# Kernel tuning notes

Measured on AMD Instinct MI355X. Metric: run time of the kernel, lower is better.

## Reference

```python
import jax, jax.numpy as jnp
import numpy as np
from jax import lax

EPS = 1e-5
B, NA, NE, NAL = 1024, 10, 10, 9

def qbn(x):
    # QBN_RM1d: divide by RMS of detached input over all dims but last
    xd = lax.stop_gradient(x)
    mean2 = jnp.mean((xd * xd).reshape(-1, xd.shape[-1]), axis=0)
    return x / jnpp_sqrt(mean2) if False else x / jnp.sqrt(mean2 + EPS)

def qrelu(x):
    # Qrelu1d: scale each 2-vector (axis -2) by mod/max(1,mod), mod from detached x
    xd = lax.stop_gradient(x)
    mod = jnp.sqrt(jnp.sum(xd * xd, axis=-2))
    coeff = mod / jnp.maximum(1.0, mod)
    return x * coeff[..., None, :]

def rcn(x, Ws):
    for W in Ws:
        x = qrelu(qbn(x @ W))
    return x

def qmerge(x):
    return jnp.sum(x * x, axis=-2)

def qmaxpool(x):
    # x: [B,A,N,2,C]; pick per-channel entity with max squared 2-norm
    xd = lax.stop_gradient(x)
    mod = jnp.sum(xd * xd, axis=-2)            # [B,A,N,C]
    idx = jnp.argmax(mod, axis=-2)             # [B,A,C]
    idxb = jnp.broadcast_to(idx[:, :, None, None, :], x.shape[:2] + (1,) + x.shape[-2:])
    return jnp.take_along_axis(x, idxb, axis=-3)[:, :, 0]   # [B,A,2,C]

def build_vec(feats, own_vec):
    # feats: [B,A,n,9]; own_vec: [B,A,2,11]
    pos = feats[..., 2:4][..., None]                          # [B,A,n,2,1]
    pos_mod = jnp.sqrt(jnp.sum(pos * pos, axis=-2))           # [B,A,n,1]
    other = jnp.concatenate([feats[..., :2], feats[..., 4:]], axis=-1)  # [B,A,n,7]
    other_mod = jnp.sqrt(2.0 * other * other)                 # repeat-2 then 2-norm = sqrt(2*x^2)
    mask = pos_mod == 0.0
    denom = jnp.where(mask, 1.0, pos_mod)
    coff = jnp.where(mask, 0.0, other_mod / denom)[..., None, :]   # [B,A,n,1,7]
    vec = pos * coff                                           # [B,A,n,2,7]
    own_mod = jnp.sqrt(jnp.sum(own_vec * own_vec, axis=-2))[:, :, None, :]  # [B,A,1,11]
    own_coff = jnp.where(mask, 0.0, own_mod / denom)[..., None, :]          # [B,A,n,1,11]
    own_vecf = pos * own_coff                                  # [B,A,n,2,11]
    return jnp.concatenate([pos, vec, own_vecf], axis=-1)      # [B,A,n,2,19]

def setup_inputs() -> dict:
    key = jax.random.key(0)
    ks = jax.random.split(key, 32)
    s = 0.1
    inp = {
        'own_feats':   jax.random.normal(ks[0], (B, NA, 11), jnp.float32),
        'enemy_feats': jax.random.normal(ks[1], (B, NA, NE, 9), jnp.float32),
        'ally_feats':  jax.random.normal(ks[2], (B, NA, NAL, 9), jnp.float32),
        'W_e1': jax.random.normal(ks[3], (19, 64), jnp.float32) * s,
        'W_e2': jax.random.normal(ks[4], (64, 64), jnp.float32) * s,
        'W_a1': jax.random.normal(ks[5], (19, 64), jnp.float32) * s,
        'W_a2': jax.random.normal(ks[6], (64, 64), jnp.float32) * s,
        'W_f1': jax.random.normal(ks[7], (64, 64), jnp.float32) * s,
        'W_f2': jax.random.normal(ks[8], (64, 64), jnp.float32) * s,
        'W_ie1': jax.random.normal(ks[9], (128, 64), jnp.float32) * s,
        'W_ie2': jax.random.normal(ks[10], (64, 64), jnp.float32) * s,
        'W_ie3': jax.random.normal(ks[11], (64, 1), jnp.float32) * s,
        'W_ia1': jax.random.normal(ks[12], (128, 64), jnp.float32) * s,
        'W_ia2': jax.random.normal(ks[13], (64, 64), jnp.float32) * s,
        'W_ia3': jax.random.normal(ks[14], (64, 1), jnp.float32) * s,
        'W_oa1': jax.random.normal(ks[15], (64, 64), jnp.float32) * s,
        'b_oa1': jnp.zeros((64,), jnp.float32),
        'W_oa2': jax.random.normal(ks[16], (64, 3), jnp.float32) * s,
        'b_oa2': jnp.zeros((3,), jnp.float32),
        'W_at1': jax.random.normal(ks[17], (128, 128), jnp.float32) * s,
        'b_at1': jnp.zeros((128,), jnp.float32),
        'W_at2': jax.random.normal(ks[18], (128, 64), jnp.float32) * s,
        'b_at2': jnp.zeros((64,), jnp.float32),
        'W_at3': jax.random.normal(ks[19], (64, 1), jnp.float32) * s,
        'b_at3': jnp.zeros((1,), jnp.float32),
    }
    return inp

def reference(own_feats, enemy_feats, ally_feats,
              W_e1, W_e2, W_a1, W_a2, W_f1, W_f2,
              W_ie1, W_ie2, W_ie3, W_ia1, W_ia2, W_ia3,
              W_oa1, b_oa1, W_oa2, b_oa2,
              W_at1, b_at1, W_at2, b_at2, W_at3, b_at3):
    Bc = own_feats.shape[0]
    own_vec = jnp.repeat(own_feats[:, :, None, :], 2, axis=2)        # [B,A,2,11]
    ev = build_vec(enemy_feats, own_vec)                              # [B,A,10,2,19]
    av = build_vec(ally_feats, own_vec)                               # [B,A,9,2,19]
    e_rc = rcn(ev, (W_e1, W_e2))                                      # [B,A,10,2,64]
    e_scalar = qmerge(e_rc)                                           # [B,A,10,64]
    a_rc = rcn(av, (W_a1, W_a2))                                      # [B,A,9,2,64]
    all_rc = jnp.concatenate([e_rc, a_rc], axis=-3)                   # [B,A,19,2,64]
    vf = rcn(qmaxpool(all_rc), (W_f1, W_f2))                          # [B,A,2,64]
    vrep = jnp.broadcast_to(vf[:, :, None], (Bc, NA, NE, 2, 64))
    cat = jnp.concatenate([vrep, e_rc], axis=-1)                      # [B,A,10,2,128]
    e_imp = rcn(cat, (W_ie1, W_ie2, W_ie3))                           # [B,A,10,2,1]
    a_imp = rcn(cat, (W_ia1, W_ia2, W_ia3))                           # (orig code also uses enemy feats here)
    move_vec = jnp.sum(jnp.concatenate([e_imp, a_imp], axis=-3), axis=-3)  # [B,A,2,1]
    sf = qmerge(vf)                                                   # [B,A,64]
    oaq = jax.nn.relu(sf @ W_oa1 + b_oa1) @ W_oa2 + b_oa2             # [B,A,3]
    mmq = oaq[:, :, 2:3]
    up = mmq + move_vec[:, :, 1, :]
    down = mmq - move_vec[:, :, 1, :]
    right = mmq + move_vec[:, :, 0, :]
    left = mmq - move_vec[:, :, 0, :]
    move_q = jnp.concatenate([up, down, right, left], axis=-1)        # [B,A,4]
    sfr = jnp.broadcast_to(sf[:, :, None, :], (Bc, NA, NE, 64))
    atf = jnp.concatenate([sfr, e_scalar], axis=-1)                   # [B,A,10,128]
    h = jax.nn.relu(atf @ W_at1 + b_at1)
    h = jax.nn.relu(h @ W_at2 + b_at2)
    aq = (h @ W_at3 + b_at3)[..., 0]                                  # [B,A,10]
    return jnp.concatenate([oaq[:, :, 0:2], move_q, aq], axis=-1)     # [B,A,16]
```

## Files before the change

### kernel.cpp

```cpp
#include <hip/hip_runtime.h>
#include <math.h>

#define BATCH 1024
#define NA 10
#define NEN 10
#define NALY 9
#define NAG (BATCH*NA)
#define NEE (NAG*NEN)
#define NAE (NAG*NALY)
#define EPSF 1e-5f

#define DOFF_SE1 0
#define DOFF_SE2 1024
#define DOFF_SA1 2048
#define DOFF_SA2 3072
#define DOFF_SF1 4096
#define DOFF_SF2 5120
#define DOFF_SIE1 6144
#define DOFF_SIE2 7168
#define DOFF_SIA1 8192
#define DOFF_SIA2 9216
#define DOFF_SIE3 10240
#define DOFF_SIA3 10368
#define NDOUBLES 16384

#define NBLK_BE (NEE/8)
#define NBLK_BA (NAE/8)
#define NBLK_PE (NEE/16)
#define NBLK_PA (NAE/16)

__device__ __forceinline__ double sum16vd(const double* __restrict__ S, int ch) {
    double s = 0.0;
#pragma unroll
    for (int r = 0; r < 16; ++r) s += S[r*64 + ch];
    return s;
}
__device__ __forceinline__ double sum16sd8(const double* __restrict__ S) {
    double s = 0.0;
#pragma unroll
    for (int r = 0; r < 16; ++r) s += S[r*8];
    return s;
}
__device__ __forceinline__ float qbn_s(const double* __restrict__ S, int ch, double invRows) {
    float m = (float)(sum16vd(S, ch)*invRows);
    return sqrtf(m + EPSF);
}
__device__ __forceinline__ void red_to_S(const double* red, double* S, int bid, int tid) {
    if (tid < 64) {
        double v = red[tid] + red[tid+64] + red[tid+128] + red[tid+192];
        atomicAdd(&S[(bid & 15)*64 + tid], v);
    }
}
__device__ __forceinline__ float pair_m2(float x0, float x1) {
    return __fadd_rn(__fmul_rn(x0,x0), __fmul_rn(x1,x1));
}

__global__ __launch_bounds__(256) void k_build_both(
    const float* __restrict__ ef, const float* __restrict__ af,
    const float* __restrict__ own,
    const float* __restrict__ We1, const float* __restrict__ Wa1,
    float* __restrict__ XE, float* __restrict__ XA,
    double* __restrict__ SE1, double* __restrict__ SA1)
{
    bool isA = (blockIdx.x >= NBLK_BE);
    int blk = isA ? (blockIdx.x - NBLK_BE) : blockIdx.x;
    const float* feats = isA ? af : ef;
    const float* W1    = isA ? Wa1 : We1;
    float* X           = isA ? XA : XE;
    double* S1         = isA ? SA1 : SE1;
    int nEntPerAgent   = isA ? NALY : NEN;

    __shared__ float wlds[19*64];
    __shared__ float gpc[16][19];
    __shared__ double red[256];
    int tid = threadIdx.x;
    for (int i = tid; i < 19*64; i += 256) wlds[i] = W1[i];
    if (tid < 152) {
        int el = tid / 19, chg = tid % 19;
        int ent = blk*8 + el;
        const float* f = feats + (size_t)ent*9;
        int agent = ent / nEntPerAgent;
        float px = f[2], py = f[3];
        float pm = sqrtf(__fadd_rn(__fmul_rn(px,px), __fmul_rn(py,py)));
        float val;
        if (chg == 0) val = 1.f;
        else if (chg < 8) {
            int j = chg - 1;
            int fi = (j < 2) ? j : (j + 2);
            float o = f[fi];
            float om = sqrtf(__fmul_rn(__fmul_rn(2.0f,o),o));
            val = (pm == 0.f) ? 0.f : __fdiv_rn(om, pm);
        } else {
            float o = own[(size_t)agent*11 + (chg-8)];
            float t = __fmul_rn(o,o);
            float om = sqrtf(__fadd_rn(t,t));
            val = (pm == 0.f) ? 0.f : __fdiv_rn(om, pm);
        }
        gpc[el*2 + 0][chg] = __fmul_rn(px, val);
        gpc[el*2 + 1][chg] = __fmul_rn(py, val);
    }
    __syncthreads();
    int l = tid >> 7, c = (tid >> 6) & 1, ch = tid & 63;
    float wreg[19];
#pragma unroll
    for (int k = 0; k < 19; ++k) wreg[k] = wlds[k*64+ch];
    double lr = 0.0;
#pragma unroll
    for (int i = 0; i < 4; ++i) {
        int el = l + 2*i;
        int ent = blk*8 + el;
        int row = el*2 + c;
        float acc = 0.f;
#pragma unroll
        for (int k = 18; k >= 0; --k) {
            acc = fmaf(gpc[row][k], wreg[k], acc);
        }
        X[(size_t)ent*128 + c*64 + ch] = acc;
        lr += (double)acc * (double)acc;
    }
    red[tid] = lr;
    __syncthreads();
    red_to_S(red, S1, blk, tid);
}

__device__ __forceinline__ void pair_layer_body(
    float* __restrict__ X, const double* __restrict__ Sin, double* __restrict__ Sout,
    const float* __restrict__ W, double invRows, int blk)
{
    __shared__ float wlds[4096];
    __shared__ float ybuf[16][132];
    __shared__ float ss[64];
    __shared__ double dredw[4][64];
    int tid = threadIdx.x;
    for (int i = tid; i < 4096; i += 256) wlds[i] = W[i];
    if (tid < 64) ss[tid] = qbn_s(Sin, tid, invRows);
    __syncthreads();
    int rl = tid >> 4;
    int ch0 = (tid & 15) * 4;
    size_t row = (size_t)blk*16 + rl;
    float4 xv0 = *(const float4*)&X[row*128 + ch0];
    float4 xv1 = *(const float4*)&X[row*128 + 64 + ch0];
    {
        float xs0[4] = {xv0.x,xv0.y,xv0.z,xv0.w};
        float xs1[4] = {xv1.x,xv1.y,xv1.z,xv1.w};
        float y0[4], y1[4];
#pragma unroll
        for (int i = 0; i < 4; ++i) {
            float s = ss[ch0+i];
            float u0 = xs0[i]/s, u1 = xs1[i]/s;
            float mod = sqrtf(pair_m2(u0,u1));
            float cf = mod / fmaxf(1.f, mod);
            y0[i] = __fmul_rn(u0,cf);
            y1[i] = __fmul_rn(u1,cf);
        }
        *(float4*)&ybuf[rl][2*ch0]     = make_float4(y0[0],y1[0],y0[1],y1[1]);
        *(float4*)&ybuf[rl][2*ch0 + 4] = make_float4(y0[2],y1[2],y0[3],y1[3]);
    }
    __syncthreads();
    float a0[4] = {0.f,0.f,0.f,0.f};
    float a1[4] = {0.f,0.f,0.f,0.f};
#pragma unroll
    for (int k = 63; k >= 1; k -= 2) {
        float4 wk  = *(const float4*)&wlds[k*64 + ch0];
        float4 wk1 = *(const float4*)&wlds[(k-1)*64 + ch0];
        float4 y4  = *(const float4*)&ybuf[rl][2*k - 2];
        float wkv[4]  = {wk.x,wk.y,wk.z,wk.w};
        float wk1v[4] = {wk1.x,wk1.y,wk1.z,wk1.w};
#pragma unroll
        for (int i = 0; i < 4; ++i) {
            a0[i] = fmaf(y4.z, wkv[i], a0[i]);
            a1[i] = fmaf(y4.w, wkv[i], a1[i]);
        }
#pragma unroll
        for (int i = 0; i < 4; ++i) {
            a0[i] = fmaf(y4.x, wk1v[i], a0[i]);
            a1[i] = fmaf(y4.y, wk1v[i], a1[i]);
        }
    }
    *(float4*)&X[row*128 + ch0]      = make_float4(a0[0],a0[1],a0[2],a0[3]);
    *(float4*)&X[row*128 + 64 + ch0] = make_float4(a1[0],a1[1],a1[2],a1[3]);
    {
        int wv = tid >> 6;
#pragma unroll
        for (int i = 0; i < 4; ++i) {
            double d = (double)a0[i]*a0[i] + (double)a1[i]*a1[i];
            d += __shfl_xor(d, 16, 64);
            d += __shfl_xor(d, 32, 64);
            if ((tid & 48) == 0) dredw[wv][ch0+i] = d;
        }
    }
    __syncthreads();
    if (tid < 64) {
        double v = dredw[0][tid] + dredw[1][tid] + dredw[2][tid] + dredw[3][tid];
        atomicAdd(&Sout[(blk & 15)*64 + tid], v);
    }
}

__global__ __launch_bounds__(256) void k_pair_both(
    float* __restrict__ XE, const double* __restrict__ SE1, double* __restrict__ SE2,
    const float* __restrict__ We2, double invRe,
    float* __restrict__ XA, const double* __restrict__ SA1, double* __restrict__ SA2,
    const float* __restrict__ Wa2, double invRa)
{
    if (blockIdx.x < NBLK_PE)
        pair_layer_body(XE, SE1, SE2, We2, invRe, blockIdx.x);
    else
        pair_layer_body(XA, SA1, SA2, Wa2, invRa, blockIdx.x - NBLK_PE);
}

__global__ __launch_bounds__(256) void k_pair_layer(
    float* __restrict__ X, const double* __restrict__ Sin, double* __restrict__ Sout,
    const float* __restrict__ W, double invRows)
{
    pair_layer_body(X, Sin, Sout, W, invRows, blockIdx.x);
}

__global__ __launch_bounds__(256) void k_finalize_pair(
    float* __restrict__ X, const double* __restrict__ S2, double invRows,
    float* __restrict__ ESC)
{
    __shared__ float ss[64];
    if (threadIdx.x < 64) ss[threadIdx.x] = qbn_s(S2, threadIdx.x, invRows);
    int t = blockIdx.x*256 + threadIdx.x;
    int rl = t >> 4;
    int ch0 = (t & 15) * 4;
    size_t base    = (size_t)rl*64 + ch0;
    size_t partner = (size_t)(rl ^ 1)*64 + ch0;
    float4 xv  = *(const float4*)&X[base];
    float4 xov = *(const float4*)&X[partner];
    __syncthreads();
    float xs[4]  = {xv.x,xv.y,xv.z,xv.w};
    float xos[4] = {xov.x,xov.y,xov.z,xov.w};
    float r[4], esc[4];
    int c = rl & 1;
#pragma unroll
    for (int i = 0; i < 4; ++i) {
        float s = ss[ch0+i];
        float u  = xs[i]/s;
        float uo = xos[i]/s;
        float u0 = (c==0) ? u : uo, u1 = (c==0) ? uo : u;
        float mod = sqrtf(pair_m2(u0,u1));
        float cf = mod / fmaxf(1.f, mod);
        r[i] = __fmul_rn(u, cf);
        if (c == 0) {
            float y1v = __fmul_rn(uo, cf);
            esc[i] = pair_m2(r[i], y1v);
        }
    }
    *(float4*)&X[base] = make_float4(r[0],r[1],r[2],r[3]);
    if (c == 0) {
        int ent = rl >> 1;
        *(float4*)&ESC[(size_t)ent*64 + ch0] = make_float4(esc[0],esc[1],esc[2],esc[3]);
    }
}

__global__ __launch_bounds__(256) void k_pool_f1(
    const float* __restrict__ XE, const float* __restrict__ XAraw,
    const double* __restrict__ SA2, double invRa,
    const float* __restrict__ Wf1, float* __restrict__ F1, double* __restrict__ Sf1)
{
    __shared__ float wlds[4096];
    __shared__ float v[4][2][64];
    __shared__ float ssa[64];
    __shared__ double red[256];
    int tid = threadIdx.x;
    for (int i = tid; i < 4096; i += 256) wlds[i] = Wf1[i];
    if (tid < 64) ssa[tid] = qbn_s(SA2, tid, invRa);
    __syncthreads();
    int grp = tid>>6, ch = tid&63;
    int agent = blockIdx.x*4 + grp;
    float best = -1.f, v0 = 0.f, v1 = 0.f;
    for (int e = 0; e < NEN; ++e) {
        size_t b = (size_t)(agent*NEN+e)*128;
        float x0 = XE[b+ch], x1 = XE[b+64+ch];
        float m2 = pair_m2(x0,x1);
        if (m2 > best) { best = m2; v0 = x0; v1 = x1; }
    }
    float sa = ssa[ch];
    for (int l = 0; l < NALY; ++l) {
        size_t b = (size_t)(agent*NALY+l)*128;
        float r0 = XAraw[b+ch], r1 = XAraw[b+64+ch];
        float u0 = r0/sa, u1 = r1/sa;
        float modf = sqrtf(pair_m2(u0,u1));
        float cff = modf / fmaxf(1.f, modf);
        float x0 = __fmul_rn(u0,cff), x1 = __fmul_rn(u1,cff);
        float m2 = pair_m2(x0,x1);
        if (m2 > best) { best = m2; v0 = x0; v1 = x1; }
    }
    v[grp][0][ch] = v0; v[grp][1][ch] = v1;
    __syncthreads();
    float a0 = 0.f, a1 = 0.f;
#pragma unroll
    for (int k = 0; k < 64; ++k) {
        float w = wlds[k*64+ch];
        a0 = fmaf(v[grp][0][k], w, a0);
        a1 = fmaf(v[grp][1][k], w, a1);
    }
    F1[(size_t)agent*128+ch] = a0; F1[(size_t)agent*128+64+ch] = a1;
    red[tid] = (double)a0*a0 + (double)a1*a1;
    __syncthreads();
    red_to_S(red, Sf1, blockIdx.x, tid);
}

__global__ __launch_bounds__(256) void k_vf_vtop(
    float* __restrict__ F1, const double* __restrict__ Sf2,
    float* __restrict__ SFb,
    const float* __restrict__ Wie1, const float* __restrict__ Wia1,
    const float* __restrict__ Wat1, const float* __restrict__ bat1,
    float* __restrict__ VTie, float* __restrict__ VTia, double invRows)
{
    __shared__ float wie[4096];
    __shared__ float wia[4096];
    __shared__ float vf[4][2][64];
    __shared__ float sfv[4][64];
    int tid = threadIdx.x;
    for (int i = tid; i < 4096; i += 256) { wie[i] = Wie1[i]; wia[i] = Wia1[i]; }
    int grp = tid>>6, ch = tid&63;
    int agent = blockIdx.x*4 + grp;
    float x0 = F1[(size_t)agent*128+ch], x1 = F1[(size_t)agent*128+64+ch];
    float s = qbn_s(Sf2, ch, invRows);
    float u0 = x0/s, u1 = x1/s;
    float mod = sqrtf(pair_m2(u0,u1));
    float cf = mod / fmaxf(1.f, mod);
    float y0 = __fmul_rn(u0,cf), y1 = __fmul_rn(u1,cf);
    vf[grp][0][ch] = y0; vf[grp][1][ch] = y1;
    float sf = pair_m2(y0,y1);
    SFb[(size_t)agent*64+ch] = sf;
    sfv[grp][ch] = sf;
    __syncthreads();
    float a0=0.f,a1=0.f,b0=0.f,b1=0.f;
    float at0 = bat1[ch], at1 = bat1[64+ch];
#pragma unroll
    for (int k = 0; k < 64; ++k) {
        float f0 = vf[grp][0][k], f1 = vf[grp][1][k];
        a0 = fmaf(f0, wie[k*64+ch], a0); a1 = fmaf(f1, wie[k*64+ch], a1);
        b0 = fmaf(f0, wia[k*64+ch], b0); b1 = fmaf(f1, wia[k*64+ch], b1);
        float sv = sfv[grp][k];
        at0 = fmaf(sv, Wat1[k*128 + ch], at0);
        at1 = fmaf(sv, Wat1[k*128 + 64 + ch], at1);
    }
    VTie[(size_t)agent*128+ch] = a0; VTie[(size_t)agent*128+64+ch] = a1;
    VTia[(size_t)agent*128+ch] = b0; VTia[(size_t)agent*128+64+ch] = b1;
    F1[(size_t)agent*128+ch] = at0; F1[(size_t)agent*128+64+ch] = at1;
}

__global__ __launch_bounds__(256) void k_imp1(
    const float* __restrict__ XE, const float* __restrict__ VT,
    const float* __restrict__ W1, float* __restrict__ XI, double* __restrict__ S1)
{
    __shared__ float wlds[4096];
    __shared__ float xt[16][68];
    __shared__ double dredw[4][64];
    int tid = threadIdx.x;
    for (int i = tid; i < 4096; i += 256) wlds[i] = W1[4096 + i];
    {
        int r = tid >> 4;
        int kq = (tid & 15) * 4;
        float4 t4 = *(const float4*)&XE[(size_t)blockIdx.x*1024 + tid*4];
        *(float4*)&xt[r][kq] = t4;
    }
    __syncthreads();
    int rl = tid >> 4;
    int ch0 = (tid & 15) * 4;
    int ent = blockIdx.x*8 + (rl >> 1);
    int c = rl & 1;
    int agent = ent / NEN;
    float4 vt = *(const float4*)&VT[(size_t)agent*128 + c*64 + ch0];
    float acc[4] = {vt.x, vt.y, vt.z, vt.w};
#pragma unroll
    for (int k = 0; k < 64; k += 4) {
        float4 x4 = *(const float4*)&xt[rl][k];
        float xk[4] = {x4.x, x4.y, x4.z, x4.w};
#pragma unroll
        for (int kk = 0; kk < 4; ++kk) {
            float4 w4 = *(const float4*)&wlds[(k+kk)*64 + ch0];
            acc[0] = fmaf(xk[kk], w4.x, acc[0]);
            acc[1] = fmaf(xk[kk], w4.y, acc[1]);
            acc[2] = fmaf(xk[kk], w4.z, acc[2]);
            acc[3] = fmaf(xk[kk], w4.w, acc[3]);
        }
    }
    *(float4*)&XI[(size_t)ent*128 + c*64 + ch0] = make_float4(acc[0],acc[1],acc[2],acc[3]);
    {
        int wv = tid >> 6;
#pragma unroll
        for (int i = 0; i < 4; ++i) {
            double d = (double)acc[i]*acc[i];
            d += __shfl_xor(d, 16, 64);
            d += __shfl_xor(d, 32, 64);
            if ((tid & 48) == 0) dredw[wv][ch0+i] = d;
        }
    }
    __syncthreads();
    if (tid < 64) {
        double v = dredw[0][tid] + dredw[1][tid] + dredw[2][tid] + dredw[3][tid];
        atomicAdd(&S1[(blockIdx.x & 15)*64 + tid], v);
    }
}

__global__ __launch_bounds__(256) void k_imp3(
    const float* __restrict__ XI, const double* __restrict__ S2,
    const float* __restrict__ W3, float* __restrict__ Z, double* __restrict__ S3,
    double invRows)
{
    __shared__ float ss[64];
    __shared__ double red4[4];
    int tid = threadIdx.x; int grp = tid>>6, ch = tid&63;
    if (tid < 64) ss[tid] = qbn_s(S2, tid, invRows);
    __syncthreads();
    float s = ss[ch];
    double w3 = (double)W3[ch];
    double lr3 = 0.0;
#pragma unroll
    for (int i = 0; i < 4; ++i) {
        int ent = blockIdx.x*16 + grp + 4*i;
        float x0 = XI[(size_t)ent*128+ch], x1 = XI[(size_t)ent*128+64+ch];
        float u0 = x0/s, u1 = x1/s;
        float mod = sqrtf(pair_m2(u0,u1));
        float cf = mod / fmaxf(1.f, mod);
        double v0 = (double)__fmul_rn(u0,cf) * w3;
        double v1 = (double)__fmul_rn(u1,cf) * w3;
#pragma unroll
        for (int m = 1; m < 64; m <<= 1) { v0 += __shfl_xor(v0,m,64); v1 += __shfl_xor(v1,m,64); }
        if (ch == 0) {
            float z0 = (float)v0, z1 = (float)v1;
            Z[(size_t)ent*2] = z0; Z[(size_t)ent*2+1] = z1;
            lr3 += (double)z0*z0 + (double)z1*z1;
        }
    }
    if (ch == 0) red4[grp] = lr3;
    __syncthreads();
    if (tid == 0) atomicAdd(&S3[(blockIdx.x & 15)*8], red4[0]+red4[1]+red4[2]+red4[3]);
}

__global__ __launch_bounds__(256) void k_final_small(
    const float* __restrict__ Zie, const float* __restrict__ Zia,
    const double* __restrict__ Sie3, const double* __restrict__ Sia3,
    const float* __restrict__ SFb,
    const float* __restrict__ Woa1, const float* __restrict__ boa1,
    const float* __restrict__ Woa2, const float* __restrict__ boa2,
    float* __restrict__ out, double invRows)
{
    __shared__ float sflds[4][64];
    int tid = threadIdx.x; int grp = tid>>6, ch = tid&63;
    int agent = blockIdx.x*4 + grp;
    float sie = sqrtf((float)(sum16sd8(Sie3)*invRows) + EPSF);
    float sia = sqrtf((float)(sum16sd8(Sia3)*invRows) + EPSF);
    double pv0 = 0.0, pv1 = 0.0;
    if (ch < NEN) {
        int ent = agent*NEN + ch;
        float z0 = Zie[(size_t)ent*2]/sie, z1 = Zie[(size_t)ent*2+1]/sie;
        float mod = sqrtf(pair_m2(z0,z1)); float cf = mod/fmaxf(1.f,mod);
        pv0 = (double)__fmul_rn(z0,cf); pv1 = (double)__fmul_rn(z1,cf);
        z0 = Zia[(size_t)ent*2]/sia; z1 = Zia[(size_t)ent*2+1]/sia;
        mod = sqrtf(pair_m2(z0,z1)); cf = mod/fmaxf(1.f,mod);
        pv0 += (double)__fmul_rn(z0,cf); pv1 += (double)__fmul_rn(z1,cf);
    }
#pragma unroll
    for (int m = 1; m < 64; m <<= 1) { pv0 += __shfl_xor(pv0,m,64); pv1 += __shfl_xor(pv1,m,64); }
    sflds[grp][ch] = SFb[(size_t)agent*64+ch];
    __syncthreads();
    double hd = (double)boa1[ch];
#pragma unroll
    for (int k = 0; k < 64; ++k) hd += (double)sflds[grp][k]*(double)Woa1[k*64+ch];
    float h = fmaxf((float)hd, 0.f);
    double q0 = (double)h*(double)Woa2[ch*3+0];
    double q1 = (double)h*(double)Woa2[ch*3+1];
    double q2 = (double)h*(double)Woa2[ch*3+2];
#pragma unroll
    for (int m = 1; m < 64; m <<= 1) { q0 += __shfl_xor(q0,m,64); q1 += __shfl_xor(q1,m,64); q2 += __shfl_xor(q2,m,64); }
    if (ch == 0) {
        float oaq0 = (float)(q0 + (double)boa2[0]);
        float oaq1 = (float)(q1 + (double)boa2[1]);
        float mmq  = (float)(q2 + (double)boa2[2]);
        float mv0 = (float)pv0, mv1 = (float)pv1;
        float* o = out + (size_t)agent*16;
        o[0] = oaq0; o[1] = oaq1;
        o[2] = mmq + mv1; o[3] = mmq - mv1;
        o[4] = mmq + mv0; o[5] = mmq - mv0;
    }
}

__global__ __launch_bounds__(256) void k_attn(
    const float* __restrict__ ATtop, const float* __restrict__ ESC,
    const float* __restrict__ W1,
    const float* __restrict__ W2, const float* __restrict__ b2,
    const float* __restrict__ W3, const float* __restrict__ b3,
    float* __restrict__ out)
{
    __shared__ float escT[64][20];
    __shared__ float h1T[128][20];
    __shared__ float h2[16][68];
    int tid = threadIdx.x;
    int row0 = blockIdx.x*16;
#pragma unroll
    for (int i = 0; i < 4; ++i) {
        int idx = tid + i*256; int r = idx>>6; int j = idx&63;
        escT[j][r] = ESC[(size_t)(row0 + r)*64 + j];
    }
    __syncthreads();
    {
        int j = tid & 127, rr = tid >> 7;
        float acc[8];
#pragma unroll
        for (int r = 0; r < 8; ++r) {
            int ent = row0 + rr*8 + r; int agent = ent/NEN;
            acc[r] = ATtop[(size_t)agent*128 + j];
        }
#pragma unroll 8
        for (int k = 0; k < 64; ++k) {
            float w = W1[(64 + k)*128 + j];
            float4 a0 = *(const float4*)&escT[k][rr*8];
            float4 a1 = *(const float4*)&escT[k][rr*8 + 4];
            acc[0] = fmaf(a0.x, w, acc[0]);
            acc[1] = fmaf(a0.y, w, acc[1]);
            acc[2] = fmaf(a0.z, w, acc[2]);
            acc[3] = fmaf(a0.w, w, acc[3]);
            acc[4] = fmaf(a1.x, w, acc[4]);
            acc[5] = fmaf(a1.y, w, acc[5]);
            acc[6] = fmaf(a1.z, w, acc[6]);
            acc[7] = fmaf(a1.w, w, acc[7]);
        }
        float4 o0 = make_float4(fmaxf(acc[0],0.f), fmaxf(acc[1],0.f),
                                fmaxf(acc[2],0.f), fmaxf(acc[3],0.f));
        float4 o1 = make_float4(fmaxf(acc[4],0.f), fmaxf(acc[5],0.f),
                                fmaxf(acc[6],0.f), fmaxf(acc[7],0.f));
        *(float4*)&h1T[j][rr*8]     = o0;
        *(float4*)&h1T[j][rr*8 + 4] = o1;
    }
    __syncthreads();
    {
        int j2 = tid & 63, rr2 = tid >> 6;
        float bb = b2[j2];
        float acc[4] = {bb, bb, bb, bb};
#pragma unroll 8
        for (int k = 0; k < 128; ++k) {
            float w = W2[k*64 + j2];
            float4 p = *(const float4*)&h1T[k][rr2*4];
            acc[0] = fmaf(p.x, w, acc[0]);
            acc[1] = fmaf(p.y, w, acc[1]);
            acc[2] = fmaf(p.z, w, acc[2]);
            acc[3] = fmaf(p.w, w, acc[3]);
        }
#pragma unroll
        for (int r = 0; r < 4; ++r) h2[rr2*4+r][j2] = fmaxf(acc[r], 0.f);
    }
    __syncthreads();
    {
        int r3 = tid >> 4, l3 = tid & 15;
        float s = 0.f;
#pragma unroll
        for (int q = 0; q < 4; ++q) s = fmaf(h2[r3][l3 + 16*q], W3[l3 + 16*q], s);
#pragma unroll
        for (int m = 1; m < 16; m <<= 1) s += __shfl_xor(s, m, 64);
        if (l3 == 0) {
            int ent = row0 + r3; int agent = ent/NEN; int e = ent%NEN;
            out[(size_t)agent*16 + 6 + e] = s + b3[0];
        }
    }
}

extern "C" void kernel_launch(void* const* d_in, const int* in_sizes, int n_in,
                              void* d_out, int out_size, void* d_ws, size_t ws_size,
                              hipStream_t stream) {
    const float* own  = (const float*)d_in[0];
    const float* ef   = (const float*)d_in[1];
    const float* af   = (const float*)d_in[2];
    const float* W_e1 = (const float*)d_in[3];
    const float* W_e2 = (const float*)d_in[4];
    const float* W_a1 = (const float*)d_in[5];
    const float* W_a2 = (const float*)d_in[6];
    const float* W_f1 = (const float*)d_in[7];
    const float* W_f2 = (const float*)d_in[8];
    const float* W_ie1= (const float*)d_in[9];
    const float* W_ie2= (const float*)d_in[10];
    const float* W_ie3= (const float*)d_in[11];
    const float* W_ia1= (const float*)d_in[12];
    const float* W_ia2= (const float*)d_in[13];
    const float* W_ia3= (const float*)d_in[14];
    const float* W_oa1= (const float*)d_in[15];
    const float* b_oa1= (const float*)d_in[16];
    const float* W_oa2= (const float*)d_in[17];
    const float* b_oa2= (const float*)d_in[18];
    const float* W_at1= (const float*)d_in[19];
    const float* b_at1= (const float*)d_in[20];
    const float* W_at2= (const float*)d_in[21];
    const float* b_at2= (const float*)d_in[22];
    const float* W_at3= (const float*)d_in[23];
    const float* b_at3= (const float*)d_in[24];
    float* out = (float*)d_out;
    float* wsf = (float*)d_ws;
    double* Sd = (double*)d_ws;

    size_t o = (size_t)NDOUBLES*2;
    float*  X_E  = wsf + o; o += (size_t)NEE*128;
    float*  X_A  = wsf + o; o += (size_t)NAE*128;
    float*  F1   = wsf + o; o += (size_t)NAG*128;
    float*  SFb  = wsf + o; o += (size_t)NAG*64;
    float*  VT_IE = wsf + o; o += (size_t)NAG*128;
    float*  VT_IA = wsf + o; o += (size_t)NAG*128;
    float*  XI   = wsf + o; o += (size_t)NEE*128;
    float*  Z_IE = wsf + o; o += (size_t)NEE*2;
    float*  Z_IA = wsf + o; o += (size_t)NEE*2;
    float*  ESC  = wsf + o; o += (size_t)NEE*64;

    double* S_E1 = Sd + DOFF_SE1;  double* S_E2 = Sd + DOFF_SE2;
    double* S_A1 = Sd + DOFF_SA1;  double* S_A2 = Sd + DOFF_SA2;
    double* S_F1 = Sd + DOFF_SF1;  double* S_F2 = Sd + DOFF_SF2;
    double* S_IE1= Sd + DOFF_SIE1; double* S_IE2= Sd + DOFF_SIE2;
    double* S_IA1= Sd + DOFF_SIA1; double* S_IA2= Sd + DOFF_SIA2;
    double* S_IE3= Sd + DOFF_SIE3; double* S_IA3= Sd + DOFF_SIA3;

    const double invRe = 1.0/(double)(NEE*2);
    const double invRa = 1.0/(double)(NAE*2);
    const double invRf = 1.0/(double)(NAG*2);

    hipMemsetAsync(Sd, 0, (size_t)NDOUBLES*sizeof(double), stream);

    k_build_both<<<NBLK_BE + NBLK_BA, 256, 0, stream>>>(
        ef, af, own, W_e1, W_a1, X_E, X_A, S_E1, S_A1);
    k_pair_both<<<NBLK_PE + NBLK_PA, 256, 0, stream>>>(
        X_E, S_E1, S_E2, W_e2, invRe, X_A, S_A1, S_A2, W_a2, invRa);
    k_finalize_pair<<<NEE*32/256, 256, 0, stream>>>(X_E, S_E2, invRe, ESC);
    k_pool_f1<<<NAG/4, 256, 0, stream>>>(X_E, X_A, S_A2, invRa, W_f1, F1, S_F1);
    k_pair_layer<<<NAG/16, 256, 0, stream>>>(F1, S_F1, S_F2, W_f2, invRf);
    k_vf_vtop<<<NAG/4, 256, 0, stream>>>(F1, S_F2, SFb, W_ie1, W_ia1,
                                         W_at1, b_at1, VT_IE, VT_IA, invRf);
    k_imp1<<<NEE/8, 256, 0, stream>>>(X_E, VT_IE, W_ie1, XI, S_IE1);
    k_pair_layer<<<NEE/16, 256, 0, stream>>>(XI, S_IE1, S_IE2, W_ie2, invRe);
    k_imp3<<<NEE/16, 256, 0, stream>>>(XI, S_IE2, W_ie3, Z_IE, S_IE3, invRe);
    k_imp1<<<NEE/8, 256, 0, stream>>>(X_E, VT_IA, W_ia1, XI, S_IA1);
    k_pair_layer<<<NEE/16, 256, 0, stream>>>(XI, S_IA1, S_IA2, W_ia2, invRe);
    k_imp3<<<NEE/16, 256, 0, stream>>>(XI, S_IA2, W_ia3, Z_IA, S_IA3, invRe);

    k_final_small<<<NAG/4, 256, 0, stream>>>(Z_IE, Z_IA, S_IE3, S_IA3, SFb,
                                             W_oa1, b_oa1, W_oa2, b_oa2, out, invRe);
    k_attn<<<NEE/16, 256, 0, stream>>>(F1, ESC, W_at1, W_at2, b_at2,
                                       W_at3, b_at3, out);
}
```

Baseline: 653.8 us.

## Fuse enemy and ally importance branches and process 32 rows per pair-layer block

The enemy and ally importance RCN chains previously ran as six sequential launches. They are now merged into one dual-weight first-layer kernel, one combined pair-layer launch and one combined final-layer kernel. The ally branch output overwrites the X_E buffer in place to avoid a second scratch buffer. Separately, each pair-layer block now handles 32 rows instead of 16, so every staged 64x64 weight tile in LDS is reused across twice as many rows. The cost is more registers and LDS per block and fewer blocks per launch, which can lower occupancy.

```diff
diff --git a/kernel.cpp b/kernel.cpp
--- a/kernel.cpp
+++ b/kernel.cpp
@@ -26,8 +26,8 @@
 
 #define NBLK_BE (NEE/8)
 #define NBLK_BA (NAE/8)
-#define NBLK_PE (NEE/16)
-#define NBLK_PA (NAE/16)
+#define NBLK_PE32 (NEE/32)
+#define NBLK_PA32 (NAE/32)
 
 __device__ __forceinline__ double sum16vd(const double* __restrict__ S, int ch) {
     double s = 0.0;
@@ -128,7 +128,7 @@
     const float* __restrict__ W, double invRows, int blk)
 {
     __shared__ float wlds[4096];
-    __shared__ float ybuf[16][132];
+    __shared__ float ybuf[32][132];
     __shared__ float ss[64];
     __shared__ double dredw[4][64];
     int tid = threadIdx.x;
@@ -137,10 +137,12 @@
     __syncthreads();
     int rl = tid >> 4;
     int ch0 = (tid & 15) * 4;
-    size_t row = (size_t)blk*16 + rl;
-    float4 xv0 = *(const float4*)&X[row*128 + ch0];
-    float4 xv1 = *(const float4*)&X[row*128 + 64 + ch0];
-    {
+#pragma unroll
+    for (int h = 0; h < 2; ++h) {
+        int r = rl + h*16;
+        size_t row = (size_t)blk*32 + r;
+        float4 xv0 = *(const float4*)&X[row*128 + ch0];
+        float4 xv1 = *(const float4*)&X[row*128 + 64 + ch0];
         float xs0[4] = {xv0.x,xv0.y,xv0.z,xv0.w};
         float xs1[4] = {xv1.x,xv1.y,xv1.z,xv1.w};
         float y0[4], y1[4];
@@ -153,37 +155,55 @@
             y0[i] = __fmul_rn(u0,cf);
             y1[i] = __fmul_rn(u1,cf);
         }
-        *(float4*)&ybuf[rl][2*ch0]     = make_float4(y0[0],y1[0],y0[1],y1[1]);
-        *(float4*)&ybuf[rl][2*ch0 + 4] = make_float4(y0[2],y1[2],y0[3],y1[3]);
+        *(float4*)&ybuf[r][2*ch0]     = make_float4(y0[0],y1[0],y0[1],y1[1]);
+        *(float4*)&ybuf[r][2*ch0 + 4] = make_float4(y0[2],y1[2],y0[3],y1[3]);
     }
     __syncthreads();
     float a0[4] = {0.f,0.f,0.f,0.f};
     float a1[4] = {0.f,0.f,0.f,0.f};
+    float c0[4] = {0.f,0.f,0.f,0.f};
+    float c1[4] = {0.f,0.f,0.f,0.f};
 #pragma unroll
     for (int k = 63; k >= 1; k -= 2) {
         float4 wk  = *(const float4*)&wlds[k*64 + ch0];
         float4 wk1 = *(const float4*)&wlds[(k-1)*64 + ch0];
-        float4 y4  = *(const float4*)&ybuf[rl][2*k - 2];
+        float4 ya  = *(const float4*)&ybuf[rl][2*k - 2];
+        float4 yb  = *(const float4*)&ybuf[rl+16][2*k - 2];
         float wkv[4]  = {wk.x,wk.y,wk.z,wk.w};
         float wk1v[4] = {wk1.x,wk1.y,wk1.z,wk1.w};
 #pragma unroll
         for (int i = 0; i < 4; ++i) {
-            a0[i] = fmaf(y4.z, wkv[i], a0[i]);
-            a1[i] = fmaf(y4.w, wkv[i], a1[i]);
+            a0[i] = fmaf(ya.z, wkv[i], a0[i]);
+            a1[i] = fmaf(ya.w, wkv[i], a1[i]);
         }
 #pragma unroll
         for (int i = 0; i < 4; ++i) {
-            a0[i] = fmaf(y4.x, wk1v[i], a0[i]);
-            a1[i] = fmaf(y4.y, wk1v[i], a1[i]);
-        }
-    }
-    *(float4*)&X[row*128 + ch0]      = make_float4(a0[0],a0[1],a0[2],a0[3]);
-    *(float4*)&X[row*128 + 64 + ch0] = make_float4(a1[0],a1[1],a1[2],a1[3]);
+            a0[i] = fmaf(ya.x, wk1v[i], a0[i]);
+            a1[i] = fmaf(ya.y, wk1v[i], a1[i]);
+        }
+#pragma unroll
+        for (int i = 0; i < 4; ++i) {
+            c0[i] = fmaf(yb.z, wkv[i], c0[i]);
+            c1[i] = fmaf(yb.w, wkv[i], c1[i]);
+        }
+#pragma unroll
+        for (int i = 0; i < 4; ++i) {
+            c0[i] = fmaf(yb.x, wk1v[i], c0[i]);
+            c1[i] = fmaf(yb.y, wk1v[i], c1[i]);
+        }
+    }
+    size_t rowA = (size_t)blk*32 + rl;
+    size_t rowB = rowA + 16;
+    *(float4*)&X[rowA*128 + ch0]      = make_float4(a0[0],a0[1],a0[2],a0[3]);
+    *(float4*)&X[rowA*128 + 64 + ch0] = make_float4(a1[0],a1[1],a1[2],a1[3]);
+    *(float4*)&X[rowB*128 + ch0]      = make_float4(c0[0],c0[1],c0[2],c0[3]);
+    *(float4*)&X[rowB*128 + 64 + ch0] = make_float4(c1[0],c1[1],c1[2],c1[3]);
     {
         int wv = tid >> 6;
 #pragma unroll
         for (int i = 0; i < 4; ++i) {
-            double d = (double)a0[i]*a0[i] + (double)a1[i]*a1[i];
+            double d = (double)a0[i]*a0[i] + (double)a1[i]*a1[i]
+                     + (double)c0[i]*c0[i] + (double)c1[i]*c1[i];
             d += __shfl_xor(d, 16, 64);
             d += __shfl_xor(d, 32, 64);
             if ((tid & 48) == 0) dredw[wv][ch0+i] = d;
@@ -202,10 +222,10 @@
     float* __restrict__ XA, const double* __restrict__ SA1, double* __restrict__ SA2,
     const float* __restrict__ Wa2, double invRa)
 {
-    if (blockIdx.x < NBLK_PE)
+    if (blockIdx.x < NBLK_PE32)
         pair_layer_body(XE, SE1, SE2, We2, invRe, blockIdx.x);
     else
-        pair_layer_body(XA, SA1, SA2, Wa2, invRa, blockIdx.x - NBLK_PE);
+        pair_layer_body(XA, SA1, SA2, Wa2, invRa, blockIdx.x - NBLK_PE32);
 }
 
 __global__ __launch_bounds__(256) void k_pair_layer(
@@ -344,15 +364,19 @@
     F1[(size_t)agent*128+ch] = at0; F1[(size_t)agent*128+64+ch] = at1;
 }
 
-__global__ __launch_bounds__(256) void k_imp1(
-    const float* __restrict__ XE, const float* __restrict__ VT,
-    const float* __restrict__ W1, float* __restrict__ XI, double* __restrict__ S1)
-{
-    __shared__ float wlds[4096];
+__global__ __launch_bounds__(256) void k_imp1_both(
+    float* __restrict__ XE,
+    const float* __restrict__ VTe, const float* __restrict__ VTa,
+    const float* __restrict__ W1e, const float* __restrict__ W1a,
+    float* __restrict__ XIe,
+    double* __restrict__ S1e, double* __restrict__ S1a)
+{
+    __shared__ float wldsE[4096];
+    __shared__ float wldsA[4096];
     __shared__ float xt[16][68];
     __shared__ double dredw[4][64];
     int tid = threadIdx.x;
-    for (int i = tid; i < 4096; i += 256) wlds[i] = W1[4096 + i];
+    for (int i = tid; i < 4096; i += 256) { wldsE[i] = W1e[4096 + i]; wldsA[i] = W1a[4096 + i]; }
     {
         int r = tid >> 4;
         int kq = (tid & 15) * 4;
@@ -365,44 +389,73 @@
     int ent = blockIdx.x*8 + (rl >> 1);
     int c = rl & 1;
     int agent = ent / NEN;
-    float4 vt = *(const float4*)&VT[(size_t)agent*128 + c*64 + ch0];
-    float acc[4] = {vt.x, vt.y, vt.z, vt.w};
+    float4 vte = *(const float4*)&VTe[(size_t)agent*128 + c*64 + ch0];
+    float4 vta = *(const float4*)&VTa[(size_t)agent*128 + c*64 + ch0];
+    float accE[4] = {vte.x, vte.y, vte.z, vte.w};
+    float accA[4] = {vta.x, vta.y, vta.z, vta.w};
 #pragma unroll
     for (int k = 0; k < 64; k += 4) {
         float4 x4 = *(const float4*)&xt[rl][k];
         float xk[4] = {x4.x, x4.y, x4.z, x4.w};
 #pragma unroll
         for (int kk = 0; kk < 4; ++kk) {
-            float4 w4 = *(const float4*)&wlds[(k+kk)*64 + ch0];
-            acc[0] = fmaf(xk[kk], w4.x, acc[0]);
-            acc[1] = fmaf(xk[kk], w4.y, acc[1]);
-            acc[2] = fmaf(xk[kk], w4.z, acc[2]);
-            acc[3] = fmaf(xk[kk], w4.w, acc[3]);
-        }
-    }
-    *(float4*)&XI[(size_t)ent*128 + c*64 + ch0] = make_float4(acc[0],acc[1],acc[2],acc[3]);
-    {
-        int wv = tid >> 6;
-#pragma unroll
-        for (int i = 0; i < 4; ++i) {
-            double d = (double)acc[i]*acc[i];
-            d += __shfl_xor(d, 16, 64);
-            d += __shfl_xor(d, 32, 64);
-            if ((tid & 48) == 0) dredw[wv][ch0+i] = d;
-        }
+            float4 we = *(const float4*)&wldsE[(k+kk)*64 + ch0];
+            accE[0] = fmaf(xk[kk], we.x, accE[0]);
+            accE[1] = fmaf(xk[kk], we.y, accE[1]);
+            accE[2] = fmaf(xk[kk], we.z, accE[2]);
+            accE[3] = fmaf(xk[kk], we.w, accE[3]);
+            float4 wa = *(const float4*)&wldsA[(k+kk)*64 + ch0];
+            accA[0] = fmaf(xk[kk], wa.x, accA[0]);
+            accA[1] = fmaf(xk[kk], wa.y, accA[1]);
+            accA[2] = fmaf(xk[kk], wa.z, accA[2]);
+            accA[3] = fmaf(xk[kk], wa.w, accA[3]);
+        }
+    }
+    *(float4*)&XIe[(size_t)ent*128 + c*64 + ch0] = make_float4(accE[0],accE[1],accE[2],accE[3]);
+    *(float4*)&XE [(size_t)ent*128 + c*64 + ch0] = make_float4(accA[0],accA[1],accA[2],accA[3]);
+    int wv = tid >> 6;
+#pragma unroll
+    for (int i = 0; i < 4; ++i) {
+        double d = (double)accE[i]*accE[i];
+        d += __shfl_xor(d, 16, 64);
+        d += __shfl_xor(d, 32, 64);
+        if ((tid & 48) == 0) dredw[wv][ch0+i] = d;
     }
     __syncthreads();
     if (tid < 64) {
         double v = dredw[0][tid] + dredw[1][tid] + dredw[2][tid] + dredw[3][tid];
-        atomicAdd(&S1[(blockIdx.x & 15)*64 + tid], v);
-    }
-}
-
-__global__ __launch_bounds__(256) void k_imp3(
-    const float* __restrict__ XI, const double* __restrict__ S2,
-    const float* __restrict__ W3, float* __restrict__ Z, double* __restrict__ S3,
-    double invRows)
-{
+        atomicAdd(&S1e[(blockIdx.x & 15)*64 + tid], v);
+    }
+    __syncthreads();
+#pragma unroll
+    for (int i = 0; i < 4; ++i) {
+        double d = (double)accA[i]*accA[i];
+        d += __shfl_xor(d, 16, 64);
+        d += __shfl_xor(d, 32, 64);
+        if ((tid & 48) == 0) dredw[wv][ch0+i] = d;
+    }
+    __syncthreads();
+    if (tid < 64) {
+        double v = dredw[0][tid] + dredw[1][tid] + dredw[2][tid] + dredw[3][tid];
+        atomicAdd(&S1a[(blockIdx.x & 15)*64 + tid], v);
+    }
+}
+
+__global__ __launch_bounds__(256) void k_imp3_both(
+    const float* __restrict__ XIe, const float* __restrict__ XIa,
+    const double* __restrict__ S2e, const double* __restrict__ S2a,
+    const float* __restrict__ W3e, const float* __restrict__ W3a,
+    float* __restrict__ Ze, float* __restrict__ Za,
+    double* __restrict__ S3e, double* __restrict__ S3a, double invRows)
+{
+    bool isA = (blockIdx.x >= (NEE/16));
+    int blk = isA ? (blockIdx.x - NEE/16) : blockIdx.x;
+    const float* XI = isA ? XIa : XIe;
+    const double* S2 = isA ? S2a : S2e;
+    const float* W3 = isA ? W3a : W3e;
+    float* Z = isA ? Za : Ze;
+    double* S3 = isA ? S3a : S3e;
+
     __shared__ float ss[64];
     __shared__ double red4[4];
     int tid = threadIdx.x; int grp = tid>>6, ch = tid&63;
@@ -413,7 +466,7 @@
     double lr3 = 0.0;
 #pragma unroll
     for (int i = 0; i < 4; ++i) {
-        int ent = blockIdx.x*16 + grp + 4*i;
+        int ent = blk*16 + grp + 4*i;
         float x0 = XI[(size_t)ent*128+ch], x1 = XI[(size_t)ent*128+64+ch];
         float u0 = x0/s, u1 = x1/s;
         float mod = sqrtf(pair_m2(u0,u1));
@@ -430,7 +483,7 @@
     }
     if (ch == 0) red4[grp] = lr3;
     __syncthreads();
-    if (tid == 0) atomicAdd(&S3[(blockIdx.x & 15)*8], red4[0]+red4[1]+red4[2]+red4[3]);
+    if (tid == 0) atomicAdd(&S3[(blk & 15)*8], red4[0]+red4[1]+red4[2]+red4[3]);
 }
 
 __global__ __launch_bounds__(256) void k_final_small(
@@ -619,19 +672,20 @@
 
     k_build_both<<<NBLK_BE + NBLK_BA, 256, 0, stream>>>(
         ef, af, own, W_e1, W_a1, X_E, X_A, S_E1, S_A1);
-    k_pair_both<<<NBLK_PE + NBLK_PA, 256, 0, stream>>>(
+    k_pair_both<<<NBLK_PE32 + NBLK_PA32, 256, 0, stream>>>(
         X_E, S_E1, S_E2, W_e2, invRe, X_A, S_A1, S_A2, W_a2, invRa);
     k_finalize_pair<<<NEE*32/256, 256, 0, stream>>>(X_E, S_E2, invRe, ESC);
     k_pool_f1<<<NAG/4, 256, 0, stream>>>(X_E, X_A, S_A2, invRa, W_f1, F1, S_F1);
-    k_pair_layer<<<NAG/16, 256, 0, stream>>>(F1, S_F1, S_F2, W_f2, invRf);
+    k_pair_layer<<<NAG/32, 256, 0, stream>>>(F1, S_F1, S_F2, W_f2, invRf);
     k_vf_vtop<<<NAG/4, 256, 0, stream>>>(F1, S_F2, SFb, W_ie1, W_ia1,
                                          W_at1, b_at1, VT_IE, VT_IA, invRf);
-    k_imp1<<<NEE/8, 256, 0, stream>>>(X_E, VT_IE, W_ie1, XI, S_IE1);
-    k_pair_layer<<<NEE/16, 256, 0, stream>>>(XI, S_IE1, S_IE2, W_ie2, invRe);
-    k_imp3<<<NEE/16, 256, 0, stream>>>(XI, S_IE2, W_ie3, Z_IE, S_IE3, invRe);
-    k_imp1<<<NEE/8, 256, 0, stream>>>(X_E, VT_IA, W_ia1, XI, S_IA1);
-    k_pair_layer<<<NEE/16, 256, 0, stream>>>(XI, S_IA1, S_IA2, W_ia2, invRe);
-    k_imp3<<<NEE/16, 256, 0, stream>>>(XI, S_IA2, W_ia3, Z_IA, S_IA3, invRe);
+    k_imp1_both<<<NEE/8, 256, 0, stream>>>(X_E, VT_IE, VT_IA, W_ie1, W_ia1,
+                                           XI, S_IE1, S_IA1);
+    k_pair_both<<<NBLK_PE32 + NBLK_PE32, 256, 0, stream>>>(
+        XI, S_IE1, S_IE2, W_ie2, invRe, X_E, S_IA1, S_IA2, W_ia2, invRe);
+    k_imp3_both<<<2*(NEE/16), 256, 0, stream>>>(XI, X_E, S_IE2, S_IA2,
+                                                W_ie3, W_ia3, Z_IE, Z_IA,
+                                                S_IE3, S_IA3, invRe);
 
     k_final_small<<<NAG/4, 256, 0, stream>>>(Z_IE, Z_IA, S_IE3, S_IA3, SFb,
                                              W_oa1, b_oa1, W_oa2, b_oa2, out, invRe);
```

Result: faster. 602.7 us (-7.8%).
